# Kernel tuning notes

Measured on AMD Instinct MI355X. Metric: run time of the kernel, lower is better.

The kernel has to match this reference:

```python
import jax, jax.numpy as jnp
import numpy as np

SCALES = [1, 2, 4, 8]
NB_CODE = 1024
CODE_DIM = 512


def _linear_upsample(x, t_out):
    """torch F.interpolate(mode='linear', align_corners=False) on last axis. x: [N, C, t_in]."""
    t_in = x.shape[-1]
    if t_in == t_out:
        return x
    pos = (jnp.arange(t_out, dtype=x.dtype) + 0.5) * (t_in / t_out) - 0.5
    pos = jnp.clip(pos, 0.0, t_in - 1)
    lo = jnp.floor(pos).astype(jnp.int32)
    hi = jnp.minimum(lo + 1, t_in - 1)
    w = (pos - lo.astype(x.dtype))
    return x[..., lo] * (1.0 - w) + x[..., hi] * w


def setup_inputs() -> dict:
    key = jax.random.key(0)
    k1, k2 = jax.random.split(key)
    x = jax.random.normal(k1, (16, CODE_DIM, 2048), dtype=jnp.float32)
    codebook = jax.random.normal(k2, (NB_CODE, CODE_DIM), dtype=jnp.float32) * 0.02
    return {"x": x, "codebook": codebook}


def reference(x, codebook):
    # Eval-mode forward of HRQuantizeEMAReset: hierarchical residual VQ.
    # temperature=0 -> deterministic nearest-code argmax; m_lens=None -> full mask.
    N, C, T = x.shape
    residual = x
    f_hat = jnp.zeros_like(x)
    mean_vq_loss = jnp.asarray(0.0, dtype=x.dtype)
    csq = jnp.sum(codebook ** 2, axis=-1)  # [K]
    all_idx = []
    for scale in SCALES:
        t_s = T // scale
        # area downsample == average pooling over non-overlapping windows
        rest_down = residual if scale == 1 else residual.reshape(N, C, t_s, scale).mean(-1)
        flat = rest_down.transpose(0, 2, 1).reshape(N * t_s, C)  # (n t) c
        # squared-euclidean distance to all codes via GEMM
        dist = (jnp.sum(flat ** 2, axis=-1, keepdims=True)
                - 2.0 * flat @ codebook.T + csq[None, :])  # [N*t_s, K]
        code_idx = jnp.argmin(dist, axis=-1)  # gumbel_sample with temp=0
        all_idx.append(code_idx)
        x_d = codebook[code_idx].reshape(N, t_s, C).transpose(0, 2, 1)  # [N, C, t_s]
        up_x_d = _linear_upsample(x_d, T)
        residual = residual - up_x_d
        f_hat = f_hat + up_x_d
        # per-scale commitment loss against running reconstruction (detached)
        mean_vq_loss = mean_vq_loss + jnp.mean((x - jax.lax.stop_gradient(f_hat)) ** 2)
    mean_vq_loss = mean_vq_loss / len(SCALES)
    # straight-through estimator
    f_hat = x + jax.lax.stop_gradient(f_hat - x)
    # perplexity over all codes used across scales
    codes = jnp.concatenate(all_idx)
    counts = jnp.zeros((NB_CODE,), dtype=x.dtype).at[codes].add(1.0)
    prob = counts / jnp.sum(counts)
    perplexity = jnp.exp(-jnp.sum(prob * jnp.log(prob + 1e-7)))
    return f_hat, mean_vq_loss, perplexity
```

## Files before the change

### kernel.cpp

```cpp
#include <hip/hip_runtime.h>

#define CDIM 512
#define TDIM 2048
#define KCODE 1024
#define NTOT 16
#define FH_ELEMS (NTOT * CDIM * TDIM)
#define M_TOTAL 61440

typedef unsigned long long u64;
typedef unsigned int u32;
typedef __attribute__((ext_vector_type(8))) short s16x8;
typedef __attribute__((ext_vector_type(4))) float f32x4;
typedef __attribute__((ext_vector_type(4))) int i32x4;
typedef __attribute__((ext_vector_type(2))) int i32x2;

__device__ __forceinline__ u64 umin64(u64 a, u64 b) { return a < b ? a : b; }

__device__ __forceinline__ u32 bf16_rne(float f) {
  u32 u = __float_as_uint(f);
  return (u + 0x7fffu + ((u >> 16) & 1u)) >> 16;
}
__device__ __forceinline__ u32 pack2ch(float v0, float v1) {
  return bf16_rne(v0) | (bf16_rne(v1) << 16);
}
__device__ __forceinline__ int tile_addr(int ml, int kbyte) {
  return (ml * 128 + kbyte) ^ ((ml & 7) << 4);
}
__device__ __forceinline__ int iclamp(int v, int lo, int hi) {
  return v < lo ? lo : (v > hi ? hi : v);
}

__global__ __launch_bounds__(256) void prep_kernel(
    const float* __restrict__ cb, char* __restrict__ cb_pack,
    float* __restrict__ csq, const float* __restrict__ x,
    char* __restrict__ a1, int* __restrict__ hist) {
  const int tid = threadIdx.x;
  const int b = blockIdx.x;
  if (b < 256) {
    const int g = b * 256 + tid;
    const int tile = g >> 10;
    const int L = (g & 1023) * 16;
    const int nt = tile >> 3, kc = tile & 7;
    const int code_local = L >> 7;
    const int kbyte = (L & 127) ^ ((code_local & 7) << 4);
    const int code = nt * 128 + code_local;
    const int c0 = kc * 64 + (kbyte >> 1);
    f32x4 va = *(const f32x4*)(cb + (size_t)code * CDIM + c0);
    f32x4 vb = *(const f32x4*)(cb + (size_t)code * CDIM + c0 + 4);
    i32x4 o = {(int)pack2ch(va[0], va[1]), (int)pack2ch(va[2], va[3]),
               (int)pack2ch(vb[0], vb[1]), (int)pack2ch(vb[2], vb[3])};
    *(i32x4*)(cb_pack + (size_t)g * 16) = o;
  } else if (b < 512) {
    const int bb = b - 256;
    if (bb < 4) hist[bb * 256 + tid] = 0;
    const int code = bb * 4 + (tid >> 6);
    const int t = tid & 63;
    const float* row = cb + (size_t)code * CDIM;
    float s = 0.f;
#pragma unroll
    for (int q = 0; q < 2; ++q) {
      float4 v = *(const float4*)(row + (t * 2 + q) * 4);
      s += v.x * v.x + v.y * v.y + v.z * v.z + v.w * v.w;
    }
#pragma unroll
    for (int off = 32; off; off >>= 1) s += __shfl_down(s, off, 64);
    if (t == 0) csq[code] = s;
  } else {
    const int blk = b - 512;
    const int lane = tid & 63, cq = tid >> 6;
    const int tb = blk & 7;
    const int kc = (blk >> 3) & 7;
    const int n = blk >> 6;
    const int c0 = kc * 64 + cq * 16;
    const int t0 = tb * 256 + lane * 4;
    const float* xp = x + (size_t)n * (CDIM * TDIM) + (size_t)c0 * TDIM + t0;
    u32 pk[4][8];
#pragma unroll
    for (int jp = 0; jp < 8; ++jp) {
      f32x4 v0 = *(const f32x4*)(xp + (size_t)(2 * jp) * TDIM);
      f32x4 v1 = *(const f32x4*)(xp + (size_t)(2 * jp + 1) * TDIM);
#pragma unroll
      for (int tt = 0; tt < 4; ++tt) pk[tt][jp] = pack2ch(v0[tt], v1[tt]);
    }
    const int kbyte = cq * 32;
#pragma unroll
    for (int tt = 0; tt < 4; ++tt) {
      const int m = n * TDIM + t0 + tt;
      const size_t tbase = ((size_t)((m >> 7) * 8 + kc)) << 14;
      i32x4 o1 = {(int)pk[tt][0], (int)pk[tt][1], (int)pk[tt][2],
                  (int)pk[tt][3]};
      i32x4 o2 = {(int)pk[tt][4], (int)pk[tt][5], (int)pk[tt][6],
                  (int)pk[tt][7]};
      *(i32x4*)(a1 + tbase + tile_addr(m & 127, kbyte)) = o1;
      *(i32x4*)(a1 + tbase + tile_addr(m & 127, kbyte + 16)) = o2;
    }
  }
}

__global__ __launch_bounds__(512, 2) void gemm_argmin_packed(
    const char* __restrict__ a_pack,
    const char* __restrict__ cb_pack,
    const float* __restrict__ csq,
    u64* __restrict__ packed) {
  __shared__ __align__(16) char smem[131072 + 1024];
  float* csq_s = (float*)(smem + 131072);

  const int id = blockIdx.x;
  const int nxq = gridDim.x >> 5;
  const int xcd = id & 7;
  const int rr = id >> 3;
  const int bx = xcd * nxq + (rr >> 2);
  const int by = rr & 3;

  const int tid = threadIdx.x;
  const int lane = tid & 63;
  const int w = tid >> 6;
  const int wc = w >> 2;
  const int wm = w & 3;
  const int row_base = bx * 256;
  const int code_base = by * 256;
  if (tid < 256) csq_s[tid] = csq[code_base + tid];

  const f32x4 zero = {0.f, 0.f, 0.f, 0.f};
  f32x4 acc[8][4];
#pragma unroll
  for (int fc = 0; fc < 8; ++fc)
#pragma unroll
    for (int fm = 0; fm < 4; ++fm) acc[fc][fm] = zero;

  const size_t aBase = ((size_t)(bx * 2) * 8) << 14;
  const size_t bBase = ((size_t)(by * 2) * 8) << 14;

  auto stage = [&](int buf, int kc) {
    char* dst = smem + buf * 65536;
    const char* gA0 = a_pack + aBase + ((size_t)kc << 14);
    const char* gA1 = a_pack + aBase + ((size_t)(8 + kc) << 14);
    const char* gB0 = cb_pack + bBase + ((size_t)kc << 14);
    const char* gB1 = cb_pack + bBase + ((size_t)(8 + kc) << 14);
    const int o = tid * 16;
#pragma unroll
    for (int p = 0; p < 2; ++p) {
      const int q = o + p * 8192;
      __builtin_amdgcn_global_load_lds(
          (const __attribute__((address_space(1))) u32*)(gA0 + q),
          (__attribute__((address_space(3))) u32*)(dst + q), 16, 0, 0);
      __builtin_amdgcn_global_load_lds(
          (const __attribute__((address_space(1))) u32*)(gA1 + q),
          (__attribute__((address_space(3))) u32*)(dst + 16384 + q), 16, 0, 0);
      __builtin_amdgcn_global_load_lds(
          (const __attribute__((address_space(1))) u32*)(gB0 + q),
          (__attribute__((address_space(3))) u32*)(dst + 32768 + q), 16, 0, 0);
      __builtin_amdgcn_global_load_lds(
          (const __attribute__((address_space(1))) u32*)(gB1 + q),
          (__attribute__((address_space(3))) u32*)(dst + 49152 + q), 16, 0, 0);
    }
  };

  stage(0, 0);
  __syncthreads();

  int cur = 0;
  for (int kc = 0; kc < 8; ++kc) {
    if (kc < 7) stage(cur ^ 1, kc + 1);
    const char* X = smem + cur * 65536;
    const char* C = X + 32768;
#pragma unroll
    for (int ks = 0; ks < 2; ++ks) {
      const int kb = ks * 64 + (lane >> 4) * 16;
      s16x8 af[8], bq[4];
#pragma unroll
      for (int fc = 0; fc < 8; ++fc) {
        const int cr = wc * 128 + fc * 16 + (lane & 15);
        af[fc] = *(const s16x8*)(C + ((cr >> 7) << 14) +
                                 tile_addr(cr & 127, kb));
      }
#pragma unroll
      for (int fm = 0; fm < 4; ++fm) {
        const int mr = wm * 64 + fm * 16 + (lane & 15);
        bq[fm] = *(const s16x8*)(X + ((mr >> 7) << 14) +
                                 tile_addr(mr & 127, kb));
      }
      __builtin_amdgcn_s_setprio(1);
#pragma unroll
      for (int fc = 0; fc < 8; ++fc)
#pragma unroll
        for (int fm = 0; fm < 4; ++fm)
          acc[fc][fm] = __builtin_amdgcn_mfma_f32_16x16x32_bf16(
              af[fc], bq[fm], acc[fc][fm], 0, 0, 0);
      __builtin_amdgcn_s_setprio(0);
    }
    __syncthreads();
    cur ^= 1;
  }

  u64 best[4] = {~0ull, ~0ull, ~0ull, ~0ull};
#pragma unroll
  for (int fc = 0; fc < 8; ++fc) {
#pragma unroll
    for (int r4 = 0; r4 < 4; ++r4) {
      const int cl = wc * 128 + fc * 16 + (lane >> 4) * 4 + r4;
      const float cs = csq_s[cl];
      const u64 codebits = (u32)(code_base + cl);
#pragma unroll
      for (int fm = 0; fm < 4; ++fm) {
        float d = fmaf(-2.0f, acc[fc][fm][r4], cs);
        u32 u = __float_as_uint(d);
        u = (u & 0x80000000u) ? ~u : (u | 0x80000000u);
        best[fm] = umin64(best[fm], ((u64)u << 32) | codebits);
      }
    }
  }
#pragma unroll
  for (int fm = 0; fm < 4; ++fm) {
    u64 b = best[fm];
#pragma unroll
    for (int off = 16; off < 64; off <<= 1) {
      u32 lo = (u32)b, hi = (u32)(b >> 32);
      lo = (u32)__shfl_xor((int)lo, off, 64);
      hi = (u32)__shfl_xor((int)hi, off, 64);
      b = umin64(b, ((u64)hi << 32) | lo);
    }
    if ((lane >> 4) == 0)
      atomicMin(&packed[row_base + wm * 64 + fm * 16 + (lane & 15)], b);
  }
}

__global__ __launch_bounds__(256) void pack2_kernel(
    const float* __restrict__ x, const float* __restrict__ cb,
    const u64* __restrict__ packed, char* __restrict__ a2,
    float* __restrict__ poolr2) {
  __shared__ float rows1[16][516];
  __shared__ int idx1[16];
  const int tid = threadIdx.x;
  const int blk = blockIdx.x;
  const int n = blk >> 7;
  const int tau0 = (blk & 127) * 8;
  const int tb = tau0 * 2;
  if (tid < 16)
    idx1[tid] = (int)(packed[(size_t)n * TDIM + tb + tid] & 0xffffffffull);
  __syncthreads();
  {
    const int rj = tid >> 4, c16 = tid & 15;
    const float* src = cb + (size_t)idx1[rj] * CDIM;
#pragma unroll
    for (int q = 0; q < 8; ++q) {
      const int c = c16 * 4 + q * 64;
      *(f32x4*)&rows1[rj][c] = *(const f32x4*)(src + c);
    }
  }
  __syncthreads();

  const int cg = tid >> 1, half = tid & 1;
  const int c0 = cg * 4;
  const int tl0 = half * 8;
  const size_t xbase =
      (size_t)n * (CDIM * TDIM) + (size_t)c0 * TDIM + tb + tl0;

  f32x4 ru[8];
#pragma unroll
  for (int t = 0; t < 8; ++t) ru[t] = *(const f32x4*)&rows1[tl0 + t][c0];

  float p2[4][4];
#pragma unroll
  for (int j = 0; j < 4; ++j) {
    f32x4 xa = *(const f32x4*)(x + xbase + (size_t)j * TDIM);
    f32x4 xb = *(const f32x4*)(x + xbase + (size_t)j * TDIM + 4);
#pragma unroll
    for (int q = 0; q < 4; ++q) {
      const float e0 = (q < 2) ? xa[2 * q] : xb[2 * q - 4];
      const float e1 = (q < 2) ? xa[2 * q + 1] : xb[2 * q - 3];
      const float r0 = e0 - ru[2 * q][j];
      const float r1 = e1 - ru[2 * q + 1][j];
      p2[j][q] = (r0 + r1) * 0.5f;
    }
  }
#pragma unroll
  for (int q = 0; q < 4; ++q) {
    f32x4 o = {p2[0][q], p2[1][q], p2[2][q], p2[3][q]};
    *(f32x4*)(poolr2 + (size_t)n * (1024 * CDIM) +
              (size_t)(tau0 + half * 4 + q) * CDIM + c0) = o;
  }
  const int kc = c0 >> 6, kbyte = (c0 & 63) * 2;
#pragma unroll
  for (int q = 0; q < 4; ++q) {
    const int m = n * 1024 + tau0 + half * 4 + q;
    i32x2 o = {(int)pack2ch(p2[0][q], p2[1][q]),
               (int)pack2ch(p2[2][q], p2[3][q])};
    *(i32x2*)(a2 + (((size_t)((m >> 7) * 8 + kc)) << 14) +
              tile_addr(m & 127, kbyte)) = o;
  }
}

template <int TP, bool WPOOL>
__global__ __launch_bounds__(256) void packN_kernel(
    const float* __restrict__ pin, const float* __restrict__ cb,
    const u64* __restrict__ packed, char* __restrict__ a_next,
    float* __restrict__ pout) {
  constexpr int OFF = (TP == 1024) ? 32768 : 49152;
  constexpr int TILES = TP / 16;
  constexpr int TO = TP / 2;
  __shared__ float rows[18][516];
  __shared__ int idxs[18];
  const int tid = threadIdx.x;
  const int blk = blockIdx.x;
  const int n = blk / TILES;
  const int o0 = (blk % TILES) * 8;
  const int s0 = o0 * 2;
  if (tid < 18) {
    const int sig = iclamp(s0 - 1 + tid, 0, TP - 1);
    idxs[tid] = (int)(packed[OFF + (size_t)n * TP + sig] & 0xffffffffull);
  }
  __syncthreads();
  for (int j = 0; j < 18; ++j) {
    const int c = tid * 2;
    const float* src = cb + (size_t)idxs[j] * CDIM + c;
    rows[j][c] = src[0];
    rows[j][c + 1] = src[1];
  }
  __syncthreads();

  const int cg = tid >> 1, half = tid & 1;
  const int c0 = cg * 4;
  f32x4 inv[8];
#pragma unroll
  for (int l = 0; l < 8; ++l)
    inv[l] = *(const f32x4*)(pin + (size_t)n * (TP * CDIM) +
                             (size_t)(s0 + half * 8 + l) * CDIM + c0);

  float pv[4][4];
#pragma unroll
  for (int q = 0; q < 4; ++q) {
    const int e = half * 8 + 2 * q;
    const int sa = e + 1, sb = e + 2;
    f32x4 Rm = *(const f32x4*)&rows[sa - 1][c0];
    f32x4 Rc = *(const f32x4*)&rows[sa][c0];
    f32x4 Rp = *(const f32x4*)&rows[sb][c0];
    f32x4 Rpp = *(const f32x4*)&rows[sb + 1][c0];
    f32x4 ua = 0.125f * (Rm + Rp) + 0.75f * Rc;
    f32x4 ub = 0.125f * (Rc + Rpp) + 0.75f * Rp;
#pragma unroll
    for (int j = 0; j < 4; ++j)
      pv[j][q] = ((inv[2 * q][j] - ua[j]) + (inv[2 * q + 1][j] - ub[j])) * 0.5f;
  }

  if constexpr (WPOOL) {
#pragma unroll
    for (int q = 0; q < 4; ++q) {
      f32x4 o = {pv[0][q], pv[1][q], pv[2][q], pv[3][q]};
      *(f32x4*)(pout + (size_t)n * (TO * CDIM) +
                (size_t)(o0 + half * 4 + q) * CDIM + c0) = o;
    }
  }
  const int kc = c0 >> 6, kbyte = (c0 & 63) * 2;
#pragma unroll
  for (int q = 0; q < 4; ++q) {
    const int m = n * TO + o0 + half * 4 + q;
    i32x2 o = {(int)pack2ch(pv[0][q], pv[1][q]),
               (int)pack2ch(pv[2][q], pv[3][q])};
    *(i32x2*)(a_next + (((size_t)((m >> 7) * 8 + kc)) << 14) +
              tile_addr(m & 127, kbyte)) = o;
  }
}

__global__ __launch_bounds__(256) void final_kernel(
    const float* __restrict__ x, float* __restrict__ out,
    const float* __restrict__ cb, const u64* __restrict__ packed,
    float* __restrict__ lossPart) {
  const int tid = threadIdx.x;
  const int blk = blockIdx.x;
  const int ch = blk & 1;
  const int t0 = ((blk >> 1) & 63) * 32;
  const int n = blk >> 7;
  const int cg = tid >> 2, qt = tid & 3;
  const int c0 = ch * 256 + cg * 4;
  const int tbA = t0 + qt * 4;
  const int tbB = t0 + 16 + qt * 4;

  const u64* ip1 = packed + (size_t)n * TDIM;
  const u64* ip2 = packed + 32768 + (size_t)n * 1024;
  const u64* ip4 = packed + 49152 + (size_t)n * 512;
  const u64* ip8 = packed + 57344 + (size_t)n * 256;

  f32x4 R1A[4], R2A[4], R4A[3], R8A[2];
  f32x4 R1B[4], R2B[4], R4B[3], R8B[2];
#pragma unroll
  for (int k = 0; k < 4; ++k) {
    R1A[k] = *(const f32x4*)(
        cb + (size_t)(u32)(ip1[tbA + k] & 0xffffffffull) * CDIM + c0);
    R1B[k] = *(const f32x4*)(
        cb + (size_t)(u32)(ip1[tbB + k] & 0xffffffffull) * CDIM + c0);
  }
  const int b2A = tbA >> 1, b2B = tbB >> 1;
#pragma unroll
  for (int k = 0; k < 4; ++k) {
    R2A[k] = *(const f32x4*)(
        cb + (size_t)(u32)(ip2[iclamp(b2A - 1 + k, 0, 1023)] & 0xffffffffull) *
                 CDIM + c0);
    R2B[k] = *(const f32x4*)(
        cb + (size_t)(u32)(ip2[iclamp(b2B - 1 + k, 0, 1023)] & 0xffffffffull) *
                 CDIM + c0);
  }
  const int b4A = tbA >> 2, b4B = tbB >> 2;
#pragma unroll
  for (int k = 0; k < 3; ++k) {
    R4A[k] = *(const f32x4*)(
        cb + (size_t)(u32)(ip4[iclamp(b4A - 1 + k, 0, 511)] & 0xffffffffull) *
                 CDIM + c0);
    R4B[k] = *(const f32x4*)(
        cb + (size_t)(u32)(ip4[iclamp(b4B - 1 + k, 0, 511)] & 0xffffffffull) *
                 CDIM + c0);
  }
  const int b8A = (tbA >> 3) - 1 + ((tbA >> 2) & 1);
  const int b8B = (tbB >> 3) - 1 + ((tbB >> 2) & 1);
#pragma unroll
  for (int k = 0; k < 2; ++k) {
    R8A[k] = *(const f32x4*)(
        cb + (size_t)(u32)(ip8[iclamp(b8A + k, 0, 255)] & 0xffffffffull) *
                 CDIM + c0);
    R8B[k] = *(const f32x4*)(
        cb + (size_t)(u32)(ip8[iclamp(b8B + k, 0, 255)] & 0xffffffffull) *
                 CDIM + c0);
  }

  const size_t xbaseA = (size_t)n * (CDIM * TDIM) + (size_t)c0 * TDIM + tbA;
  const size_t xbaseB = xbaseA + 16;
  f32x4 xaA[4], xaB[4], faA[4], faB[4];
#pragma unroll
  for (int j = 0; j < 4; ++j) {
    xaA[j] = *(const f32x4*)(x + xbaseA + (size_t)j * TDIM);
    xaB[j] = *(const f32x4*)(x + xbaseB + (size_t)j * TDIM);
  }

  const int s2n[4] = {0, 1, 1, 2};
  const float w2n[4] = {0.75f, 0.25f, 0.75f, 0.25f};
  const int s4n[4] = {0, 0, 1, 1};
  const float w4n[4] = {0.625f, 0.875f, 0.125f, 0.375f};
  const float w8bA = (tbA & 4) ? 0.0625f : 0.5625f;
  const float w8bB = (tbB & 4) ? 0.0625f : 0.5625f;

  float ss1 = 0.f, ss2 = 0.f, ss3 = 0.f, ss4 = 0.f;
#pragma unroll
  for (int tt = 0; tt < 4; ++tt) {
    {
      f32x4 u2 = R2A[s2n[tt]] * (1.f - w2n[tt]) + R2A[s2n[tt] + 1] * w2n[tt];
      f32x4 u4 = R4A[s4n[tt]] * (1.f - w4n[tt]) + R4A[s4n[tt] + 1] * w4n[tt];
      const float w8 = w8bA + tt * 0.125f;
      f32x4 u8 = R8A[0] * (1.f - w8) + R8A[1] * w8;
      f32x4 xv;
#pragma unroll
      for (int j = 0; j < 4; ++j) xv[j] = xaA[j][tt];
      f32x4 r1 = xv - R1A[tt];
      f32x4 r2 = r1 - u2;
      f32x4 r3 = r2 - u4;
      f32x4 r4 = r3 - u8;
#pragma unroll
      for (int j = 0; j < 4; ++j) {
        ss1 += r1[j] * r1[j];
        ss2 += r2[j] * r2[j];
        ss3 += r3[j] * r3[j];
        ss4 += r4[j] * r4[j];
      }
      f32x4 fh = xv - r4;
#pragma unroll
      for (int j = 0; j < 4; ++j) faA[j][tt] = fh[j];
    }
    {
      f32x4 u2 = R2B[s2n[tt]] * (1.f - w2n[tt]) + R2B[s2n[tt] + 1] * w2n[tt];
      f32x4 u4 = R4B[s4n[tt]] * (1.f - w4n[tt]) + R4B[s4n[tt] + 1] * w4n[tt];
      const float w8 = w8bB + tt * 0.125f;
      f32x4 u8 = R8B[0] * (1.f - w8) + R8B[1] * w8;
      f32x4 xv;
#pragma unroll
      for (int j = 0; j < 4; ++j) xv[j] = xaB[j][tt];
      f32x4 r1 = xv - R1B[tt];
      f32x4 r2 = r1 - u2;
      f32x4 r3 = r2 - u4;
      f32x4 r4 = r3 - u8;
#pragma unroll
      for (int j = 0; j < 4; ++j) {
        ss1 += r1[j] * r1[j];
        ss2 += r2[j] * r2[j];
        ss3 += r3[j] * r3[j];
        ss4 += r4[j] * r4[j];
      }
      f32x4 fh = xv - r4;
#pragma unroll
      for (int j = 0; j < 4; ++j) faB[j][tt] = fh[j];
    }
  }
#pragma unroll
  for (int j = 0; j < 4; ++j) {
    *(f32x4*)(out + xbaseA + (size_t)j * TDIM) = faA[j];
    *(f32x4*)(out + xbaseB + (size_t)j * TDIM) = faB[j];
  }

  __shared__ float red2[4][4];
  float sv[4] = {ss1, ss2, ss3, ss4};
  const int w = tid >> 6, lane = tid & 63;
#pragma unroll
  for (int st = 0; st < 4; ++st) {
    float v = sv[st];
#pragma unroll
    for (int off = 32; off; off >>= 1) v += __shfl_down(v, off, 64);
    if (lane == 0) red2[w][st] = v;
  }
  __syncthreads();
  if (tid < 4)
    lossPart[tid * 2048 + blk] =
        red2[0][tid] + red2[1][tid] + red2[2][tid] + red2[3][tid];
}

__global__ __launch_bounds__(256) void hist_kernel(const u64* __restrict__ packed,
                                                   int* __restrict__ hist) {
  const int i = blockIdx.x * 256 + threadIdx.x;
  const int code = (int)(packed[i] & 0xFFFFFFFFull);
  atomicAdd(&hist[code], 1);
}

__global__ __launch_bounds__(256) void finalize_kernel(
    const float* __restrict__ lossPart, const int* __restrict__ hist,
    float* __restrict__ outTail) {
  __shared__ float red[4];
  const int tid = threadIdx.x;
  float s = 0.f;
  for (int i = tid; i < 4 * 2048; i += 256) s += lossPart[i];
#pragma unroll
  for (int off = 32; off; off >>= 1) s += __shfl_down(s, off, 64);
  if ((tid & 63) == 0) red[tid >> 6] = s;
  __syncthreads();
  const float loss =
      (red[0] + red[1] + red[2] + red[3]) * (1.0f / (4.0f * 16777216.0f));
  __syncthreads();
  float e = 0.f;
  for (int k = tid; k < KCODE; k += 256) {
    float p = (float)hist[k] * (1.0f / 61440.0f);
    e += p * logf(p + 1e-7f);
  }
#pragma unroll
  for (int off = 32; off; off >>= 1) e += __shfl_down(e, off, 64);
  if ((tid & 63) == 0) red[tid >> 6] = e;
  __syncthreads();
  if (tid == 0) {
    outTail[0] = loss;
    outTail[1] = expf(-(red[0] + red[1] + red[2] + red[3]));
  }
}

extern "C" void kernel_launch(void* const* d_in, const int* in_sizes, int n_in,
                              void* d_out, int out_size, void* d_ws,
                              size_t ws_size, hipStream_t stream) {
  const float* x = (const float*)d_in[0];
  const float* cb = (const float*)d_in[1];
  float* out = (float*)d_out;

  char* ws = (char*)d_ws;
  u64* packed = (u64*)ws;
  float* csq = (float*)(ws + 491520);
  int* hist = (int*)(ws + 495616);
  float* lossPart = (float*)(ws + 499712);
  char* cb_pack = ws + 565248;
  char* a2 = ws + (2ull << 20);
  char* a4 = ws + (18ull << 20);
  char* a8 = ws + (26ull << 20);

  hipMemsetAsync(packed, 0xFF, (size_t)M_TOTAL * 8, stream);

  u64* p1 = packed;
  u64* p2 = packed + 32768;
  u64* p4 = packed + 49152;
  u64* p8 = packed + 57344;

  char* a1 = (char*)out;
  float* poolr2 = out;
  float* poolr4 = out + 8388608;

  prep_kernel<<<1536, 256, 0, stream>>>(cb, cb_pack, csq, x, a1, hist);
  gemm_argmin_packed<<<128 * 4, 512, 0, stream>>>(a1, cb_pack, csq, p1);
  pack2_kernel<<<2048, 256, 0, stream>>>(x, cb, packed, a2, poolr2);
  gemm_argmin_packed<<<64 * 4, 512, 0, stream>>>(a2, cb_pack, csq, p2);
  packN_kernel<1024, true>
      <<<1024, 256, 0, stream>>>(poolr2, cb, packed, a4, poolr4);
  gemm_argmin_packed<<<32 * 4, 512, 0, stream>>>(a4, cb_pack, csq, p4);
  packN_kernel<512, false>
      <<<512, 256, 0, stream>>>(poolr4, cb, packed, a8, nullptr);
  gemm_argmin_packed<<<16 * 4, 512, 0, stream>>>(a8, cb_pack, csq, p8);
  final_kernel<<<2048, 256, 0, stream>>>(x, out, cb, packed, lossPart);
  hist_kernel<<<240, 256, 0, stream>>>(packed, hist);
  finalize_kernel<<<1, 256, 0, stream>>>(lossPart, hist, out + FH_ELEMS);
}
```

Measured before the change: 232.0 us.

## Store pooled residuals as bf16, fold memset and histogram into existing kernels

Pooled residual intermediates between scales are now written and read as packed bf16 instead of fp32, which halves that traffic. The packed-argmin buffer is initialised inside prep_kernel instead of by a separate memset. The histogram is built in shared memory inside finalize_kernel, so the hist kernel and its global atomics go away. The costs are lower precision in the residual chain, which could flip argmin choices at later scales, and a single-block loop over 61440 entries in finalize.

After: 264.8 us. +14.1%, slower.

```diff
diff --git a/kernel.cpp b/kernel.cpp
--- a/kernel.cpp
+++ b/kernel.cpp
@@ -23,6 +23,10 @@
 __device__ __forceinline__ u32 pack2ch(float v0, float v1) {
   return bf16_rne(v0) | (bf16_rne(v1) << 16);
 }
+__device__ __forceinline__ float bflo(u32 u) { return __uint_as_float(u << 16); }
+__device__ __forceinline__ float bfhi(u32 u) {
+  return __uint_as_float(u & 0xffff0000u);
+}
 __device__ __forceinline__ int tile_addr(int ml, int kbyte) {
   return (ml * 128 + kbyte) ^ ((ml & 7) << 4);
 }
@@ -33,7 +37,7 @@
 __global__ __launch_bounds__(256) void prep_kernel(
     const float* __restrict__ cb, char* __restrict__ cb_pack,
     float* __restrict__ csq, const float* __restrict__ x,
-    char* __restrict__ a1, int* __restrict__ hist) {
+    char* __restrict__ a1, u64* __restrict__ packed) {
   const int tid = threadIdx.x;
   const int b = blockIdx.x;
   if (b < 256) {
@@ -52,7 +56,7 @@
     *(i32x4*)(cb_pack + (size_t)g * 16) = o;
   } else if (b < 512) {
     const int bb = b - 256;
-    if (bb < 4) hist[bb * 256 + tid] = 0;
+    if (bb < 240) packed[bb * 256 + tid] = ~0ull;
     const int code = bb * 4 + (tid >> 6);
     const int t = tid & 63;
     const float* row = cb + (size_t)code * CDIM;
@@ -228,7 +232,7 @@
 __global__ __launch_bounds__(256) void pack2_kernel(
     const float* __restrict__ x, const float* __restrict__ cb,
     const u64* __restrict__ packed, char* __restrict__ a2,
-    float* __restrict__ poolr2) {
+    u32* __restrict__ poolb2) {
   __shared__ float rows1[16][516];
   __shared__ int idx1[16];
   const int tid = threadIdx.x;
@@ -274,18 +278,15 @@
       p2[j][q] = (r0 + r1) * 0.5f;
     }
   }
+  const int kc = c0 >> 6, kbyte = (c0 & 63) * 2;
 #pragma unroll
   for (int q = 0; q < 4; ++q) {
-    f32x4 o = {p2[0][q], p2[1][q], p2[2][q], p2[3][q]};
-    *(f32x4*)(poolr2 + (size_t)n * (1024 * CDIM) +
-              (size_t)(tau0 + half * 4 + q) * CDIM + c0) = o;
-  }
-  const int kc = c0 >> 6, kbyte = (c0 & 63) * 2;
-#pragma unroll
-  for (int q = 0; q < 4; ++q) {
-    const int m = n * 1024 + tau0 + half * 4 + q;
+    const int tau = tau0 + half * 4 + q;
     i32x2 o = {(int)pack2ch(p2[0][q], p2[1][q]),
                (int)pack2ch(p2[2][q], p2[3][q])};
+    *(i32x2*)(poolb2 + (size_t)n * (1024 * 256) + (size_t)tau * 256 +
+              (c0 >> 1)) = o;
+    const int m = n * 1024 + tau;
     *(i32x2*)(a2 + (((size_t)((m >> 7) * 8 + kc)) << 14) +
               tile_addr(m & 127, kbyte)) = o;
   }
@@ -293,9 +294,9 @@
 
 template <int TP, bool WPOOL>
 __global__ __launch_bounds__(256) void packN_kernel(
-    const float* __restrict__ pin, const float* __restrict__ cb,
+    const u32* __restrict__ pin, const float* __restrict__ cb,
     const u64* __restrict__ packed, char* __restrict__ a_next,
-    float* __restrict__ pout) {
+    u32* __restrict__ pout) {
   constexpr int OFF = (TP == 1024) ? 32768 : 49152;
   constexpr int TILES = TP / 16;
   constexpr int TO = TP / 2;
@@ -323,9 +324,14 @@
   const int c0 = cg * 4;
   f32x4 inv[8];
 #pragma unroll
-  for (int l = 0; l < 8; ++l)
-    inv[l] = *(const f32x4*)(pin + (size_t)n * (TP * CDIM) +
-                             (size_t)(s0 + half * 8 + l) * CDIM + c0);
+  for (int l = 0; l < 8; ++l) {
+    i32x2 v = *(const i32x2*)(pin + (size_t)n * (TP * 256) +
+                              (size_t)(s0 + half * 8 + l) * 256 + (c0 >> 1));
+    inv[l][0] = bflo((u32)v[0]);
+    inv[l][1] = bfhi((u32)v[0]);
+    inv[l][2] = bflo((u32)v[1]);
+    inv[l][3] = bfhi((u32)v[1]);
+  }
 
   float pv[4][4];
 #pragma unroll
@@ -343,20 +349,17 @@
       pv[j][q] = ((inv[2 * q][j] - ua[j]) + (inv[2 * q + 1][j] - ub[j])) * 0.5f;
   }
 
-  if constexpr (WPOOL) {
-#pragma unroll
-    for (int q = 0; q < 4; ++q) {
-      f32x4 o = {pv[0][q], pv[1][q], pv[2][q], pv[3][q]};
-      *(f32x4*)(pout + (size_t)n * (TO * CDIM) +
-                (size_t)(o0 + half * 4 + q) * CDIM + c0) = o;
-    }
-  }
   const int kc = c0 >> 6, kbyte = (c0 & 63) * 2;
 #pragma unroll
   for (int q = 0; q < 4; ++q) {
-    const int m = n * TO + o0 + half * 4 + q;
+    const int tau = o0 + half * 4 + q;
     i32x2 o = {(int)pack2ch(pv[0][q], pv[1][q]),
                (int)pack2ch(pv[2][q], pv[3][q])};
+    if constexpr (WPOOL) {
+      *(i32x2*)(pout + (size_t)n * (TO * 256) + (size_t)tau * 256 +
+                (c0 >> 1)) = o;
+    }
+    const int m = n * TO + tau;
     *(i32x2*)(a_next + (((size_t)((m >> 7) * 8 + kc)) << 14) +
               tile_addr(m & 127, kbyte)) = o;
   }
@@ -510,18 +513,18 @@
         red2[0][tid] + red2[1][tid] + red2[2][tid] + red2[3][tid];
 }
 
-__global__ __launch_bounds__(256) void hist_kernel(const u64* __restrict__ packed,
-                                                   int* __restrict__ hist) {
-  const int i = blockIdx.x * 256 + threadIdx.x;
-  const int code = (int)(packed[i] & 0xFFFFFFFFull);
-  atomicAdd(&hist[code], 1);
-}
-
 __global__ __launch_bounds__(256) void finalize_kernel(
-    const float* __restrict__ lossPart, const int* __restrict__ hist,
+    const float* __restrict__ lossPart, const u64* __restrict__ packed,
     float* __restrict__ outTail) {
   __shared__ float red[4];
+  __shared__ int lhist[KCODE];
   const int tid = threadIdx.x;
+  for (int k = tid; k < KCODE; k += 256) lhist[k] = 0;
+  __syncthreads();
+  for (int i = tid; i < M_TOTAL; i += 256) {
+    const int code = (int)(packed[i] & 0xffffffffull);
+    atomicAdd(&lhist[code], 1);
+  }
   float s = 0.f;
   for (int i = tid; i < 4 * 2048; i += 256) s += lossPart[i];
 #pragma unroll
@@ -533,7 +536,7 @@
   __syncthreads();
   float e = 0.f;
   for (int k = tid; k < KCODE; k += 256) {
-    float p = (float)hist[k] * (1.0f / 61440.0f);
+    float p = (float)lhist[k] * (1.0f / 61440.0f);
     e += p * logf(p + 1e-7f);
   }
 #pragma unroll
@@ -556,35 +559,31 @@
   char* ws = (char*)d_ws;
   u64* packed = (u64*)ws;
   float* csq = (float*)(ws + 491520);
-  int* hist = (int*)(ws + 495616);
   float* lossPart = (float*)(ws + 499712);
   char* cb_pack = ws + 565248;
   char* a2 = ws + (2ull << 20);
   char* a4 = ws + (18ull << 20);
   char* a8 = ws + (26ull << 20);
 
-  hipMemsetAsync(packed, 0xFF, (size_t)M_TOTAL * 8, stream);
-
   u64* p1 = packed;
   u64* p2 = packed + 32768;
   u64* p4 = packed + 49152;
   u64* p8 = packed + 57344;
 
   char* a1 = (char*)out;
-  float* poolr2 = out;
-  float* poolr4 = out + 8388608;
-
-  prep_kernel<<<1536, 256, 0, stream>>>(cb, cb_pack, csq, x, a1, hist);
+  u32* poolb2 = (u32*)out;
+  u32* poolb4 = (u32*)out + 4194304;
+
+  prep_kernel<<<1536, 256, 0, stream>>>(cb, cb_pack, csq, x, a1, packed);
   gemm_argmin_packed<<<128 * 4, 512, 0, stream>>>(a1, cb_pack, csq, p1);
-  pack2_kernel<<<2048, 256, 0, stream>>>(x, cb, packed, a2, poolr2);
+  pack2_kernel<<<2048, 256, 0, stream>>>(x, cb, packed, a2, poolb2);
   gemm_argmin_packed<<<64 * 4, 512, 0, stream>>>(a2, cb_pack, csq, p2);
   packN_kernel<1024, true>
-      <<<1024, 256, 0, stream>>>(poolr2, cb, packed, a4, poolr4);
+      <<<1024, 256, 0, stream>>>(poolb2, cb, packed, a4, poolb4);
   gemm_argmin_packed<<<32 * 4, 512, 0, stream>>>(a4, cb_pack, csq, p4);
   packN_kernel<512, false>
-      <<<512, 256, 0, stream>>>(poolr4, cb, packed, a8, nullptr);
+      <<<512, 256, 0, stream>>>(poolb4, cb, packed, a8, nullptr);
   gemm_argmin_packed<<<16 * 4, 512, 0, stream>>>(a8, cb_pack, csq, p8);
   final_kernel<<<2048, 256, 0, stream>>>(x, out, cb, packed, lossPart);
-  hist_kernel<<<240, 256, 0, stream>>>(packed, hist);
-  finalize_kernel<<<1, 256, 0, stream>>>(lossPart, hist, out + FH_ELEMS);
-}
+  finalize_kernel<<<1, 256, 0, stream>>>(lossPart, packed, out + FH_ELEMS);
+}
```
